# Performance work log

Measured on AMD Instinct MI355X. Metric: run time of the kernel, lower is better.

## Reference

```python
import jax, jax.numpy as jnp
import numpy as np

CAPS = 16          # num_capsules
DIM = 16           # capsule_dim
NUM_ROUTING = 3
L2_EPS = 1e-12     # tf.nn.l2_normalize epsilon


def setup_inputs() -> dict:
    key = jax.random.key(0)
    k1, k2 = jax.random.split(key)
    inputs = jax.random.normal(k1, (16, 64, 64, 128), dtype=jnp.float32)
    # Conv2D kernel, HWIO layout, fan-in scaled like glorot-ish init
    kernel = jax.random.normal(k2, (3, 3, 128, CAPS * DIM), dtype=jnp.float32) * 0.03
    bias = jnp.zeros((CAPS * DIM,), dtype=jnp.float32)
    return {"inputs": inputs, "kernel": kernel, "bias": bias}


def reference(inputs, kernel, bias):
    # Conv2D(caps*dim, 3x3, padding='same', activation='relu'), channels_last
    x = jax.lax.conv_general_dilated(
        inputs, kernel, window_strides=(1, 1), padding="SAME",
        dimension_numbers=("NHWC", "HWIO", "NHWC"))
    x = jax.nn.relu(x + bias)
    B, H, W, _ = x.shape
    x = x.reshape(B, H * W, CAPS, DIM)            # (B, N, C, D)
    b = jnp.zeros((B, H * W, CAPS), dtype=x.dtype)
    v = None
    for _ in range(NUM_ROUTING):
        c = jax.nn.softmax(b, axis=-1)             # over capsules
        s = jnp.einsum("bnc,bncd->bcd", c, x)      # weighted sum over spatial
        # tf.nn.l2_normalize along last axis
        v = s * jax.lax.rsqrt(jnp.maximum(jnp.sum(s * s, axis=-1, keepdims=True), L2_EPS))
        b = b + jnp.einsum("bncd,bcd->bnc", x, v)  # agreement update
    # tile v over spatial dims: (B,1,1,C*D) -> (B,H,W,C*D)
    out = jnp.broadcast_to(v.reshape(B, 1, 1, CAPS * DIM), (B, H, W, CAPS * DIM))
    return out
```

## Files before the change

kernel.cpp:

```cpp
#include <hip/hip_runtime.h>
#include <hip/hip_bf16.h>

typedef unsigned short u16;
typedef unsigned int   u32;

typedef __bf16 bf16x8 __attribute__((ext_vector_type(8)));
typedef float  f32x4  __attribute__((ext_vector_type(4)));

__device__ __forceinline__ u16 f2b(float f) {
    __hip_bfloat16 h = __float2bfloat16(f);
    u16 u; __builtin_memcpy(&u, &h, 2); return u;
}
__device__ __forceinline__ float blo(u32 u) { return __uint_as_float(u << 16); }
__device__ __forceinline__ float bhi(u32 u) { return __uint_as_float(u & 0xffff0000u); }

__global__ void k_prep(const float* __restrict__ wk,
                       u16* __restrict__ BF, float* __restrict__ stats) {
    int bx = blockIdx.x, tid = threadIdx.x;
    if (bx < 1152) {
        int t = bx * 256 + tid;
        int j  = t & 7;
        int n  = (t >> 3) & 255;
        int q  = (t >> 11) & 3;
        int kk = (t >> 13) & 3;
        int p  = t >> 15;
        BF[t] = f2b(wk[(p * 128 + kk * 32 + q * 8 + j) * 256 + n]);
    } else {
        stats[(bx - 1152) * 256 + tid] = 0.f;
    }
}

__launch_bounds__(256, 2)
__global__ void k_conv(const float* __restrict__ in, const u16* __restrict__ BF,
                       const float* __restrict__ bias,
                       u16* __restrict__ X, float* __restrict__ s0) {
    __shared__ u16 ldsA[12672];
    const int t = threadIdx.x;
    const int lane = t & 63, wid = t >> 6;
    const int q = lane >> 4, l15 = lane & 15;
    const int bb = blockIdx.x >> 6;
    const int h  = blockIdx.x & 63;
    const int wn0 = wid << 6;

#define STAGE(S) { \
    const int sb0 = wid * 396; \
    _Pragma("unroll") for (int i = 0; i < 7; ++i) { \
        int slot = sb0 + i * 64 + lane; \
        if (i < 6 || lane < 12) { \
            int pr = slot / 528; int rem = slot - pr * 528; \
            int wp = rem >> 3, cs = rem & 7; \
            int gc = (S) * 8 + (cs ^ (wp & 7)); \
            int y = h + pr - 1, x = wp - 1; \
            u16 ov[8]; \
            if (y >= 0 && y < 64 && x >= 0 && x < 64) { \
                const float4* s4 = (const float4*)(in + \
                    (((bb * 64 + y) * 64 + x) * 128 + gc * 8)); \
                float4 f0 = s4[0], f1 = s4[1]; \
                ov[0]=f2b(f0.x); ov[1]=f2b(f0.y); ov[2]=f2b(f0.z); ov[3]=f2b(f0.w); \
                ov[4]=f2b(f1.x); ov[5]=f2b(f1.y); ov[6]=f2b(f1.z); ov[7]=f2b(f1.w); \
            } else { \
                _Pragma("unroll") for (int j = 0; j < 8; ++j) ov[j] = 0; \
            } \
            uint4 wv; __builtin_memcpy(&wv, ov, 16); \
            *(uint4*)((char*)ldsA + slot * 16) = wv; \
        } \
    } }

#define LOADB(B, P, S) { \
    _Pragma("unroll") for (int kk = 0; kk < 2; ++kk) \
    _Pragma("unroll") for (int ni = 0; ni < 4; ++ni) \
        B[kk * 4 + ni] = *(const bf16x8*)(BFl + (P) * 32768 + \
                                          ((S) * 2 + kk) * 8192 + ni * 128); }

#define COMPP(B, DH, DW) { \
    _Pragma("unroll") for (int kk = 0; kk < 2; ++kk) { \
        bf16x8 af[4]; \
        _Pragma("unroll") for (int mi = 0; mi < 4; ++mi) { \
            int wp = mi * 16 + l15 + (DW); \
            int swz = (kk * 4 + q) ^ (wp & 7); \
            af[mi] = *(const bf16x8*)((const char*)ldsA + \
                (((DH) * 528 + wp * 8 + swz) << 4)); \
        } \
        _Pragma("unroll") for (int mi = 0; mi < 4; ++mi) \
        _Pragma("unroll") for (int ni = 0; ni < 4; ++ni) \
            acc[mi][ni] = __builtin_amdgcn_mfma_f32_16x16x32_bf16( \
                af[mi], B[kk * 4 + ni], acc[mi][ni], 0, 0, 0); } }

    const u16* BFl = BF + (q * 2048 + (wn0 + l15) * 8);

    f32x4 zero = {0.f, 0.f, 0.f, 0.f};
    f32x4 acc[4][4];
    #pragma unroll
    for (int mi = 0; mi < 4; ++mi)
        #pragma unroll
        for (int ni = 0; ni < 4; ++ni) acc[mi][ni] = zero;

    bf16x8 B0[8], B1[8];

    STAGE(0);
    __syncthreads();
    LOADB(B0, 0, 0);
    LOADB(B1, 1, 0); COMPP(B0, 0, 0);
    LOADB(B0, 2, 0); COMPP(B1, 0, 1);
    LOADB(B1, 3, 0); COMPP(B0, 0, 2);
    LOADB(B0, 4, 0); COMPP(B1, 1, 0);
    LOADB(B1, 5, 0); COMPP(B0, 1, 1);
    LOADB(B0, 6, 0); COMPP(B1, 1, 2);
    LOADB(B1, 7, 0); COMPP(B0, 2, 0);
    LOADB(B0, 8, 0); COMPP(B1, 2, 1);
    COMPP(B0, 2, 2);
    __syncthreads();

    STAGE(1);
    __syncthreads();
    LOADB(B0, 0, 1);
    LOADB(B1, 1, 1); COMPP(B0, 0, 0);
    LOADB(B0, 2, 1); COMPP(B1, 0, 1);
    LOADB(B1, 3, 1); COMPP(B0, 0, 2);
    LOADB(B0, 4, 1); COMPP(B1, 1, 0);
    LOADB(B1, 5, 1); COMPP(B0, 1, 1);
    LOADB(B0, 6, 1); COMPP(B1, 1, 2);
    LOADB(B1, 7, 1); COMPP(B0, 2, 0);
    LOADB(B0, 8, 1); COMPP(B1, 2, 1);
    COMPP(B0, 2, 2);

    float bv[4];
    #pragma unroll
    for (int ni = 0; ni < 4; ++ni) bv[ni] = bias[wn0 + ni * 16 + l15];
    float colsum[4] = {0.f, 0.f, 0.f, 0.f};
    u16* xrow = X + (((bb << 12) + (h << 6) + q * 4) * 256) + wn0 + l15;
    #pragma unroll
    for (int mi = 0; mi < 4; ++mi) {
        #pragma unroll
        for (int rr = 0; rr < 4; ++rr) {
            u16* xp = xrow + (mi * 16 + rr) * 256;
            #pragma unroll
            for (int ni = 0; ni < 4; ++ni) {
                float v = acc[mi][ni][rr] + bv[ni];
                v = v > 0.f ? v : 0.f;
                xp[ni * 16] = f2b(v);
                colsum[ni] += v;
            }
        }
    }
    #pragma unroll
    for (int ni = 0; ni < 4; ++ni) {
        float c = colsum[ni];
        c += __shfl_xor(c, 16);
        c += __shfl_xor(c, 32);
        if (lane < 16) atomicAdd(&s0[bb * 256 + wn0 + ni * 16 + l15], c);
    }
#undef STAGE
#undef LOADB
#undef COMPP
}

__launch_bounds__(256, 4)
__global__ void k_pass(const u16* __restrict__ X, const float* __restrict__ Sa,
                       const float* __restrict__ Sb, float* __restrict__ Sout,
                       int use2) {
    __shared__ float vs[272];
    __shared__ float red[4 * 272];
    const int t = threadIdx.x, b = blockIdx.y, chunk = blockIdx.x;
    const int c = t & 15, nl = t >> 4;
    const int lane = t & 63, wid = t >> 6;
    {
        float sa = Sa[b * 256 + t];
        float ss = sa * sa;
        #pragma unroll
        for (int off = 1; off < 16; off <<= 1) ss += __shfl_xor(ss, off);
        ss = ss < 1e-12f ? 1e-12f : ss;
        float vv = sa / sqrtf(ss);
        if (use2) {
            float sb = Sb[b * 256 + t];
            float s2v = sb * sb;
            #pragma unroll
            for (int off = 1; off < 16; off <<= 1) s2v += __shfl_xor(s2v, off);
            s2v = s2v < 1e-12f ? 1e-12f : s2v;
            vv += sb / sqrtf(s2v);
        }
        vs[(t >> 4) * 17 + (t & 15)] = vv;
    }
    const u16* xbase = X + ((b << 12) + chunk * 64 + nl) * 256 + c * 16;
    uint4 pa[8];
    #pragma unroll
    for (int r = 0; r < 4; ++r) {
        pa[2 * r]     = ((const uint4*)(xbase + r * 4096))[0];
        pa[2 * r + 1] = ((const uint4*)(xbase + r * 4096))[1];
    }
    __syncthreads();
    float vr[16];
    #pragma unroll
    for (int d = 0; d < 16; ++d) vr[d] = vs[c * 17 + d];

    float acc[16];
    #pragma unroll
    for (int d = 0; d < 16; ++d) acc[d] = 0.f;

    #pragma unroll
    for (int r = 0; r < 4; ++r) {
        u32 us[8];
        __builtin_memcpy(us, &pa[2 * r], 32);
        float xf[16];
        #pragma unroll
        for (int j = 0; j < 8; ++j) { xf[2*j] = blo(us[j]); xf[2*j+1] = bhi(us[j]); }
        float bvv = 0.f;
        #pragma unroll
        for (int d = 0; d < 16; ++d) bvv += xf[d] * vr[d];
        float e = __expf(bvv);
        float sm = e;
        #pragma unroll
        for (int off = 1; off < 16; off <<= 1) sm += __shfl_xor(sm, off);
        float w = e / sm;
        #pragma unroll
        for (int d = 0; d < 16; ++d) acc[d] += w * xf[d];
    }
    #pragma unroll
    for (int d = 0; d < 16; ++d) {
        acc[d] += __shfl_xor(acc[d], 16);
        acc[d] += __shfl_xor(acc[d], 32);
    }
    if (lane < 16) {
        #pragma unroll
        for (int d = 0; d < 16; ++d) red[wid * 272 + lane * 17 + d] = acc[d];
    }
    __syncthreads();
    {
        int c2 = t >> 4, d2 = t & 15;
        float tot = red[c2 * 17 + d2]       + red[272 + c2 * 17 + d2]
                  + red[544 + c2 * 17 + d2] + red[816 + c2 * 17 + d2];
        atomicAdd(&Sout[b * 256 + t], tot);
    }
}

__launch_bounds__(256, 4)
__global__ void k_bcast(const float* __restrict__ S, float* __restrict__ Out) {
    __shared__ float vls[256];
    int t = threadIdx.x, bx = blockIdx.x, b = blockIdx.y;
    float s = S[b * 256 + t];
    float ss = s * s;
    #pragma unroll
    for (int off = 1; off < 16; off <<= 1) ss += __shfl_xor(ss, off);
    ss = ss < 1e-12f ? 1e-12f : ss;
    vls[t] = s / sqrtf(ss);
    __syncthreads();
    float4 myv = ((const float4*)vls)[t & 63];
    float4* o = (float4*)Out + (long)b * 262144 + bx * 4096;
    #pragma unroll
    for (int j = 0; j < 16; ++j) o[j * 256 + t] = myv;
}

extern "C" void kernel_launch(void* const* d_in, const int* in_sizes, int n_in,
                              void* d_out, int out_size, void* d_ws, size_t ws_size,
                              hipStream_t stream) {
    const float* in   = (const float*)d_in[0];
    const float* wk   = (const float*)d_in[1];
    const float* bias = (const float*)d_in[2];
    float* out = (float*)d_out;
    char* ws = (char*)d_ws;

    const size_t OFF_BF  = 0;
    const size_t OFF_X   = 589824;
    const size_t OFF_ST  = 34144256;
    const size_t NEEDED  = OFF_ST + 3 * 16384;
    if (ws_size < NEEDED) return;

    u16* BF  = (u16*)(ws + OFF_BF);
    u16* X   = (u16*)(ws + OFF_X);
    float* s0 = (float*)(ws + OFF_ST);
    float* s2 = s0 + 4096;
    float* s3 = s2 + 4096;

    k_prep <<<1200, 256, 0, stream>>>(wk, BF, s0);
    k_conv <<<1024, 256, 0, stream>>>(in, BF, bias, X, s0);
    k_pass <<<dim3(64, 16), 256, 0, stream>>>(X, s0, s0, s2, 0);
    k_pass <<<dim3(64, 16), 256, 0, stream>>>(X, s0, s2, s3, 1);
    k_bcast<<<dim3(64, 16), 256, 0, stream>>>(s3, out);
}
```

Measured before the change: 158.7 us.

## Shrink conv B-register buffers, raise occupancy, and make halo loads branchless

The conv kernel's launch bound goes from 2 to 3 blocks per SM. The double-buffered weight fragments are halved by splitting each tap's K into two 4-fragment chunks and pipelining them separately, which cuts register pressure enough to fit the higher occupancy. The input staging replaces the bounds-check branch with a clamped address load multiplied by a 0/1 mask, so every lane issues the same loads. The finer pipeline gives less lookahead per load, and the masked path performs extra loads for halo lanes.

New measurement: 181.9 us. 1.15x slower.

```diff
diff --git a/kernel.cpp b/kernel.cpp
--- a/kernel.cpp
+++ b/kernel.cpp
@@ -30,7 +30,7 @@
     }
 }
 
-__launch_bounds__(256, 2)
+__launch_bounds__(256, 3)
 __global__ void k_conv(const float* __restrict__ in, const u16* __restrict__ BF,
                        const float* __restrict__ bias,
                        u16* __restrict__ X, float* __restrict__ s0) {
@@ -51,40 +51,58 @@
             int wp = rem >> 3, cs = rem & 7; \
             int gc = (S) * 8 + (cs ^ (wp & 7)); \
             int y = h + pr - 1, x = wp - 1; \
+            int inb = ((unsigned)y < 64u) & ((unsigned)x < 64u); \
+            int ys = inb ? y : 0, xs = inb ? x : 0; \
+            const float4* s4 = (const float4*)(in + \
+                (((bb * 64 + ys) * 64 + xs) * 128 + gc * 8)); \
+            float4 f0 = s4[0], f1 = s4[1]; \
+            float zf = inb ? 1.f : 0.f; \
             u16 ov[8]; \
-            if (y >= 0 && y < 64 && x >= 0 && x < 64) { \
-                const float4* s4 = (const float4*)(in + \
-                    (((bb * 64 + y) * 64 + x) * 128 + gc * 8)); \
-                float4 f0 = s4[0], f1 = s4[1]; \
-                ov[0]=f2b(f0.x); ov[1]=f2b(f0.y); ov[2]=f2b(f0.z); ov[3]=f2b(f0.w); \
-                ov[4]=f2b(f1.x); ov[5]=f2b(f1.y); ov[6]=f2b(f1.z); ov[7]=f2b(f1.w); \
-            } else { \
-                _Pragma("unroll") for (int j = 0; j < 8; ++j) ov[j] = 0; \
-            } \
+            ov[0]=f2b(f0.x*zf); ov[1]=f2b(f0.y*zf); ov[2]=f2b(f0.z*zf); ov[3]=f2b(f0.w*zf); \
+            ov[4]=f2b(f1.x*zf); ov[5]=f2b(f1.y*zf); ov[6]=f2b(f1.z*zf); ov[7]=f2b(f1.w*zf); \
             uint4 wv; __builtin_memcpy(&wv, ov, 16); \
             *(uint4*)((char*)ldsA + slot * 16) = wv; \
         } \
     } }
 
-#define LOADB(B, P, S) { \
-    _Pragma("unroll") for (int kk = 0; kk < 2; ++kk) \
+#define LOADB4(B, P, S, KK) { \
     _Pragma("unroll") for (int ni = 0; ni < 4; ++ni) \
-        B[kk * 4 + ni] = *(const bf16x8*)(BFl + (P) * 32768 + \
-                                          ((S) * 2 + kk) * 8192 + ni * 128); }
-
-#define COMPP(B, DH, DW) { \
-    _Pragma("unroll") for (int kk = 0; kk < 2; ++kk) { \
-        bf16x8 af[4]; \
-        _Pragma("unroll") for (int mi = 0; mi < 4; ++mi) { \
-            int wp = mi * 16 + l15 + (DW); \
-            int swz = (kk * 4 + q) ^ (wp & 7); \
-            af[mi] = *(const bf16x8*)((const char*)ldsA + \
-                (((DH) * 528 + wp * 8 + swz) << 4)); \
-        } \
-        _Pragma("unroll") for (int mi = 0; mi < 4; ++mi) \
-        _Pragma("unroll") for (int ni = 0; ni < 4; ++ni) \
-            acc[mi][ni] = __builtin_amdgcn_mfma_f32_16x16x32_bf16( \
-                af[mi], B[kk * 4 + ni], acc[mi][ni], 0, 0, 0); } }
+        B[ni] = *(const bf16x8*)(BFl + (P) * 32768 + \
+                                 ((S) * 2 + (KK)) * 8192 + ni * 128); }
+
+#define COMP4(B, DH, DW, KK) { \
+    bf16x8 af[4]; \
+    _Pragma("unroll") for (int mi = 0; mi < 4; ++mi) { \
+        int wp = mi * 16 + l15 + (DW); \
+        int swz = ((KK) * 4 + q) ^ (wp & 7); \
+        af[mi] = *(const bf16x8*)((const char*)ldsA + \
+            (((DH) * 528 + wp * 8 + swz) << 4)); \
+    } \
+    _Pragma("unroll") for (int mi = 0; mi < 4; ++mi) \
+    _Pragma("unroll") for (int ni = 0; ni < 4; ++ni) \
+        acc[mi][ni] = __builtin_amdgcn_mfma_f32_16x16x32_bf16( \
+            af[mi], B[ni], acc[mi][ni], 0, 0, 0); }
+
+#define HALF(S) { \
+    LOADB4(B0, 0, S, 0); \
+    LOADB4(B1, 0, S, 1); COMP4(B0, 0, 0, 0); \
+    LOADB4(B0, 1, S, 0); COMP4(B1, 0, 0, 1); \
+    LOADB4(B1, 1, S, 1); COMP4(B0, 0, 1, 0); \
+    LOADB4(B0, 2, S, 0); COMP4(B1, 0, 1, 1); \
+    LOADB4(B1, 2, S, 1); COMP4(B0, 0, 2, 0); \
+    LOADB4(B0, 3, S, 0); COMP4(B1, 0, 2, 1); \
+    LOADB4(B1, 3, S, 1); COMP4(B0, 1, 0, 0); \
+    LOADB4(B0, 4, S, 0); COMP4(B1, 1, 0, 1); \
+    LOADB4(B1, 4, S, 1); COMP4(B0, 1, 1, 0); \
+    LOADB4(B0, 5, S, 0); COMP4(B1, 1, 1, 1); \
+    LOADB4(B1, 5, S, 1); COMP4(B0, 1, 2, 0); \
+    LOADB4(B0, 6, S, 0); COMP4(B1, 1, 2, 1); \
+    LOADB4(B1, 6, S, 1); COMP4(B0, 2, 0, 0); \
+    LOADB4(B0, 7, S, 0); COMP4(B1, 2, 0, 1); \
+    LOADB4(B1, 7, S, 1); COMP4(B0, 2, 1, 0); \
+    LOADB4(B0, 8, S, 0); COMP4(B1, 2, 1, 1); \
+    LOADB4(B1, 8, S, 1); COMP4(B0, 2, 2, 0); \
+                         COMP4(B1, 2, 2, 1); }
 
     const u16* BFl = BF + (q * 2048 + (wn0 + l15) * 8);
 
@@ -95,34 +113,16 @@
         #pragma unroll
         for (int ni = 0; ni < 4; ++ni) acc[mi][ni] = zero;
 
-    bf16x8 B0[8], B1[8];
+    bf16x8 B0[4], B1[4];
 
     STAGE(0);
     __syncthreads();
-    LOADB(B0, 0, 0);
-    LOADB(B1, 1, 0); COMPP(B0, 0, 0);
-    LOADB(B0, 2, 0); COMPP(B1, 0, 1);
-    LOADB(B1, 3, 0); COMPP(B0, 0, 2);
-    LOADB(B0, 4, 0); COMPP(B1, 1, 0);
-    LOADB(B1, 5, 0); COMPP(B0, 1, 1);
-    LOADB(B0, 6, 0); COMPP(B1, 1, 2);
-    LOADB(B1, 7, 0); COMPP(B0, 2, 0);
-    LOADB(B0, 8, 0); COMPP(B1, 2, 1);
-    COMPP(B0, 2, 2);
+    HALF(0);
     __syncthreads();
 
     STAGE(1);
     __syncthreads();
-    LOADB(B0, 0, 1);
-    LOADB(B1, 1, 1); COMPP(B0, 0, 0);
-    LOADB(B0, 2, 1); COMPP(B1, 0, 1);
-    LOADB(B1, 3, 1); COMPP(B0, 0, 2);
-    LOADB(B0, 4, 1); COMPP(B1, 1, 0);
-    LOADB(B1, 5, 1); COMPP(B0, 1, 1);
-    LOADB(B0, 6, 1); COMPP(B1, 1, 2);
-    LOADB(B1, 7, 1); COMPP(B0, 2, 0);
-    LOADB(B0, 8, 1); COMPP(B1, 2, 1);
-    COMPP(B0, 2, 2);
+    HALF(1);
 
     float bv[4];
     #pragma unroll
@@ -151,8 +151,9 @@
         if (lane < 16) atomicAdd(&s0[bb * 256 + wn0 + ni * 16 + l15], c);
     }
 #undef STAGE
-#undef LOADB
-#undef COMPP
+#undef LOADB4
+#undef COMP4
+#undef HALF
 }
 
 __launch_bounds__(256, 4)
```
